# Optimization experiments

Hardware: AMD Instinct MI355X
Metric: run time of the kernel (lower is better)

Reference implementation:

```python
import jax, jax.numpy as jnp
import numpy as np


def to_float8(x, exp_bits=4, mant_bits=3):
    # Faithful port of the torch to_float8: clamp exponent, round mantissa.
    max_exp = 2 ** (exp_bits - 1) - 1
    scale = 2.0 ** mant_bits
    sign = jnp.sign(x)
    xa = jnp.abs(x)
    e = jnp.clip(jnp.floor(jnp.log2(xa + 1e-08)), -max_exp, max_exp)
    p = jnp.exp2(e)
    mant_q = jnp.round((xa / p - 1.0) * scale) / scale
    return sign * (1.0 + mant_q) * p


def setup_inputs() -> dict:
    key = jax.random.key(0)
    k0, k1, k2, k3, k4 = jax.random.split(key, 5)
    Bz, Din, L, N, Dout = 32, 512, 512, 512, 512
    u = jax.random.normal(k0, (Bz, Din, L), jnp.float32)
    # |A| < 1 for a stable length-512 recurrence
    A_diag = jax.random.uniform(k1, (N,), jnp.float32, 0.0, 0.9)
    B = jax.random.normal(k2, (N, Din), jnp.float32) * (1.0 / np.sqrt(Din))
    C = jax.random.normal(k3, (Dout, N), jnp.float32) * (1.0 / np.sqrt(N))
    D = jax.random.normal(k4, (Dout, Din), jnp.float32) * (1.0 / np.sqrt(Din))
    return {"u": u, "A_diag": A_diag, "B": B, "C": C, "D": D}


def reference(u, A_diag, B, C, D):
    int_bits, mant_bits = 4, 3
    q = lambda t: to_float8(t, int_bits, mant_bits)
    A_q = q(A_diag)[None, :]          # [1, N]
    B_q, C_q, D_q = q(B), q(C), q(D)
    Bt = B_q.T                         # [Din, N]
    # row_checksum(B_q.t()): append column of row sums -> constant across steps
    right_cs = jnp.concatenate([Bt, Bt.sum(axis=1, keepdims=True)], axis=1)  # [Din, N+1]
    Bz, Din, L = u.shape
    N = A_diag.shape[0]
    u_t = jnp.transpose(u, (2, 0, 1))  # [L, Bz, Din]

    def step(state, ut):
        # col_checksum(ut): append row of column sums
        left_cs = jnp.concatenate([ut, ut.sum(axis=0, keepdims=True)], axis=0)  # [Bz+1, Din]
        prod_cs = left_cs @ right_cs                 # [Bz+1, N+1] checksum-padded matmul
        right_term = prod_cs[:-1, :-1]               # ut @ B_q.T  (ABFT mask is discarded in forward)
        state_q = q(state * A_q + right_term)        # [Bz, N]
        y = q(state_q @ C_q.T + ut @ D_q.T)          # [Bz, Dout]
        return state_q, y

    state0 = jnp.zeros((Bz, N), u.dtype)
    _, Y = jax.lax.scan(step, state0, u_t)           # [L, Bz, Dout]
    return jnp.transpose(Y, (1, 2, 0))               # [Bz, Dout, L]
```

## Files before the change

### kernel.cpp

```cpp
#include <hip/hip_runtime.h>
#include <hip/hip_bf16.h>


#define DINX 512
#define LSEQ 512
#define NDIM 512

__device__ __forceinline__ float q8(float x) {
    float xa = fabsf(x);
    float w  = __fadd_rn(xa, 1e-8f);
    int e = (int)((__float_as_uint(w) >> 23) & 0xFFu) - 127;
    e = e < -7 ? -7 : (e > 7 ? 7 : e);
    float p    = __int_as_float((unsigned)((e + 127) << 23));
    float invp = __int_as_float((unsigned)((127 - e) << 23));
    float t  = __fmul_rn(__fsub_rn(__fmul_rn(xa, invp), 1.0f), 8.0f);
    float m  = __fmul_rn(rintf(t), 0.125f);
    float r  = __fmul_rn(__fadd_rn(1.0f, m), p);
    return copysignf(r, x);
}

__global__ void quantk(const float* __restrict__ in, float* __restrict__ out, int n) {
    int i = blockIdx.x * blockDim.x + threadIdx.x;
    if (i < n) out[i] = q8(in[i]);
}

__global__ __launch_bounds__(256) void quantT3(const float* __restrict__ B,
                                               const float* __restrict__ C,
                                               const float* __restrict__ D,
                                               float* __restrict__ Bqt,
                                               float* __restrict__ Cqt,
                                               float* __restrict__ Dqt) {
    __shared__ float tl[32][33];
    const float* in = blockIdx.z == 0 ? B : (blockIdx.z == 1 ? C : D);
    float* out      = blockIdx.z == 0 ? Bqt : (blockIdx.z == 1 ? Cqt : Dqt);
    const int r0 = blockIdx.y * 32, c0 = blockIdx.x * 32;
    const int x = threadIdx.x & 31, y = threadIdx.x >> 5;
#pragma unroll
    for (int i = 0; i < 32; i += 8)
        tl[y + i][x] = q8(in[(r0 + y + i) * 512 + c0 + x]);
    __syncthreads();
#pragma unroll
    for (int i = 0; i < 32; i += 8)
        out[(c0 + y + i) * 512 + r0 + x] = tl[x][y + i];
}

__device__ __forceinline__ void gemm_pass(const float* __restrict__ X,
                                          const float* __restrict__ W,
                                          int m0, int n0, int KTOT,
                                          float (&acc)[2][4][2][4],
                                          float (*Xs)[128], float (*Ws)[128],
                                          int tid) {
    const int tx = tid & 15, ty = tid >> 4;
    const int srow = tid >> 4, sseg4 = (tid & 15) * 4;
    const float* xp = X + (size_t)srow * 512 + m0 + sseg4;
    const float* wp = W + (size_t)srow * 512 + n0 + sseg4;
    for (int k0 = 0; k0 < KTOT; k0 += 16) {
        float4 x0 = *(const float4*)xp;
        float4 x1 = *(const float4*)(xp + 64);
        float4 w0 = *(const float4*)wp;
        float4 w1 = *(const float4*)(wp + 64);
        xp += 16 * 512; wp += 16 * 512;
        __syncthreads();
        *(float4*)&Xs[srow][sseg4]      = x0;
        *(float4*)&Xs[srow][64 + sseg4] = x1;
        *(float4*)&Ws[srow][sseg4]      = w0;
        *(float4*)&Ws[srow][64 + sseg4] = w1;
        __syncthreads();
#pragma unroll
        for (int k = 0; k < 16; ++k) {
            float a[2][4], b[2][4];
            *(float4*)&a[0][0] = *(const float4*)&Xs[k][tx * 4];
            *(float4*)&a[1][0] = *(const float4*)&Xs[k][64 + tx * 4];
            *(float4*)&b[0][0] = *(const float4*)&Ws[k][ty * 4];
            *(float4*)&b[1][0] = *(const float4*)&Ws[k][64 + ty * 4];
#pragma unroll
            for (int p = 0; p < 2; ++p)
#pragma unroll
                for (int i = 0; i < 4; ++i)
#pragma unroll
                    for (int q = 0; q < 2; ++q)
#pragma unroll
                        for (int j = 0; j < 4; ++j)
                            acc[p][i][q][j] = fmaf(a[p][i], b[q][j], acc[p][i][q][j]);
        }
    }
}

__global__ __launch_bounds__(256) void gemm_R(const float* __restrict__ u,
                                              const float* __restrict__ Bqt,
                                              float* __restrict__ R) {
    __shared__ float Xs[16][128];
    __shared__ float Ws[16][128];
    const int b  = blockIdx.z;
    const int t0 = blockIdx.x * 128, n0 = blockIdx.y * 128;
    const int tid = threadIdx.x;
    const int tx = tid & 15, ty = tid >> 4;
    const float* ub = u + (size_t)b * (DINX * LSEQ);
    float acc[2][4][2][4] = {};
    gemm_pass(ub, Bqt, t0, n0, DINX, acc, Xs, Ws, tid);
    float* Rb = R + (size_t)b * (LSEQ * NDIM);
#pragma unroll
    for (int p = 0; p < 2; ++p)
#pragma unroll
        for (int i = 0; i < 4; ++i) {
            float* row = Rb + (size_t)(t0 + p * 64 + tx * 4 + i) * NDIM + n0;
            *(float4*)(row + ty * 4)      = make_float4(acc[p][i][0][0], acc[p][i][0][1],
                                                        acc[p][i][0][2], acc[p][i][0][3]);
            *(float4*)(row + 64 + ty * 4) = make_float4(acc[p][i][1][0], acc[p][i][1][1],
                                                        acc[p][i][1][2], acc[p][i][1][3]);
        }
}

__global__ __launch_bounds__(128) void recur(const float* __restrict__ R,
                                             const float* __restrict__ Aq,
                                             float* __restrict__ S) {
    __shared__ float tile[16][132];
    const int b  = blockIdx.x;
    const int n0 = blockIdx.y * 128;
    const int n  = threadIdx.x;
    const float a = Aq[n0 + n];
    const float* Rb = R + (size_t)b * (LSEQ * NDIM) + n0;
    float* Sb = S + (size_t)b * (NDIM * LSEQ) + (size_t)n0 * LSEQ;
    float s = 0.0f;
    const int c = (n & 3) * 4;
    const int rbase = n >> 2;
    for (int t0 = 0; t0 < LSEQ; t0 += 16) {
#pragma unroll
        for (int tt = 0; tt < 16; ++tt) {
            float r = Rb[(size_t)(t0 + tt) * NDIM + n];
            s = q8(__fadd_rn(__fmul_rn(s, a), r));
            tile[tt][n] = s;
        }
        __syncthreads();
#pragma unroll
        for (int p = 0; p < 4; ++p) {
            int row = p * 32 + rbase;
            float4 v = make_float4(tile[c + 0][row], tile[c + 1][row],
                                   tile[c + 2][row], tile[c + 3][row]);
            *(float4*)(Sb + (size_t)row * LSEQ + t0 + c) = v;
        }
        __syncthreads();
    }
}

__global__ __launch_bounds__(256) void gemm_Y(const float* __restrict__ u,
                                              const float* __restrict__ S,
                                              const float* __restrict__ Cqt,
                                              const float* __restrict__ Dqt,
                                              float* __restrict__ Y) {
    __shared__ float Xs[16][128];
    __shared__ float Ws[16][128];
    const int b  = blockIdx.z;
    const int t0 = blockIdx.x * 128, o0 = blockIdx.y * 128;
    const int tid = threadIdx.x;
    const int tx = tid & 15, ty = tid >> 4;
    const float* Sb = S + (size_t)b * (NDIM * LSEQ);
    const float* ub = u + (size_t)b * (DINX * LSEQ);
    float acc[2][4][2][4] = {};
    float c1[2][4][2][4];
    gemm_pass(Sb, Cqt, t0, o0, NDIM, acc, Xs, Ws, tid);
#pragma unroll
    for (int p = 0; p < 2; ++p)
#pragma unroll
        for (int i = 0; i < 4; ++i)
#pragma unroll
            for (int q = 0; q < 2; ++q)
#pragma unroll
                for (int j = 0; j < 4; ++j) {
                    c1[p][i][q][j] = acc[p][i][q][j];
                    acc[p][i][q][j] = 0.0f;
                }
    gemm_pass(ub, Dqt, t0, o0, DINX, acc, Xs, Ws, tid);

    float* Yb = Y + (size_t)b * (NDIM * LSEQ);
#pragma unroll
    for (int q = 0; q < 2; ++q)
#pragma unroll
        for (int j = 0; j < 4; ++j) {
            float y0[4], y1[4];
#pragma unroll
            for (int i = 0; i < 4; ++i) {
                y0[i] = q8(__fadd_rn(c1[0][i][q][j], acc[0][i][q][j]));
                y1[i] = q8(__fadd_rn(c1[1][i][q][j], acc[1][i][q][j]));
            }
            float* row = Yb + (size_t)(o0 + q * 64 + ty * 4 + j) * LSEQ + t0;
            *(float4*)(row + tx * 4)      = make_float4(y0[0], y0[1], y0[2], y0[3]);
            *(float4*)(row + 64 + tx * 4) = make_float4(y1[0], y1[1], y1[2], y1[3]);
        }
}

extern "C" void kernel_launch(void* const* d_in, const int* in_sizes, int n_in,
                              void* d_out, int out_size, void* d_ws, size_t ws_size,
                              hipStream_t stream) {
    const float* u = (const float*)d_in[0];
    const float* A = (const float*)d_in[1];
    const float* B = (const float*)d_in[2];
    const float* C = (const float*)d_in[3];
    const float* D = (const float*)d_in[4];

    float* ws  = (float*)d_ws;
    float* Aq  = ws;
    float* Bqt = Aq + 512;
    float* Cqt = Bqt + 262144;
    float* Dqt = Cqt + 262144;
    float* R   = Dqt + 262144;
    float* S   = R + 8388608;
    float* Y   = (float*)d_out;

    quantk<<<2, 256, 0, stream>>>(A, Aq, 512);
    quantT3<<<dim3(16, 16, 3), 256, 0, stream>>>(B, C, D, Bqt, Cqt, Dqt);

    gemm_R<<<dim3(4, 4, 32), 256, 0, stream>>>(u, Bqt, R);
    recur<<<dim3(32, 4), 128, 0, stream>>>(R, Aq, S);
    gemm_Y<<<dim3(4, 4, 32), 256, 0, stream>>>(u, S, Cqt, Dqt, Y);
}
```

Measured before the change: 405.1 us.

## Double-buffer GEMM shared tiles and split recurrence into smaller blocks

Converts the shared GEMM inner loop to a double-buffered scheme: the next K-tile is prefetched into registers while the current tile is computed, then written to the alternate shared buffer, leaving one barrier per tile. It also halves the recurrence block width to 64 channels, doubling the block count to spread the serial scan across more compute units. The cost is doubled shared memory per GEMM block, which may lower occupancy.

```diff
diff --git a/kernel.cpp b/kernel.cpp
--- a/kernel.cpp
+++ b/kernel.cpp
@@ -44,6 +44,28 @@
         out[(c0 + y + i) * 512 + r0 + x] = tl[x][y + i];
 }
 
+__device__ __forceinline__ void tile16(const float (*Xs)[128], const float (*Ws)[128],
+                                       int base, int tx, int ty,
+                                       float (&acc)[2][4][2][4]) {
+#pragma unroll
+    for (int k = 0; k < 16; ++k) {
+        float a[2][4], b[2][4];
+        *(float4*)&a[0][0] = *(const float4*)&Xs[base + k][tx * 4];
+        *(float4*)&a[1][0] = *(const float4*)&Xs[base + k][64 + tx * 4];
+        *(float4*)&b[0][0] = *(const float4*)&Ws[base + k][ty * 4];
+        *(float4*)&b[1][0] = *(const float4*)&Ws[base + k][64 + ty * 4];
+#pragma unroll
+        for (int p = 0; p < 2; ++p)
+#pragma unroll
+            for (int i = 0; i < 4; ++i)
+#pragma unroll
+                for (int q = 0; q < 2; ++q)
+#pragma unroll
+                    for (int j = 0; j < 4; ++j)
+                        acc[p][i][q][j] = fmaf(a[p][i], b[q][j], acc[p][i][q][j]);
+    }
+}
+
 __device__ __forceinline__ void gemm_pass(const float* __restrict__ X,
                                           const float* __restrict__ W,
                                           int m0, int n0, int KTOT,
@@ -54,7 +76,8 @@
     const int srow = tid >> 4, sseg4 = (tid & 15) * 4;
     const float* xp = X + (size_t)srow * 512 + m0 + sseg4;
     const float* wp = W + (size_t)srow * 512 + n0 + sseg4;
-    for (int k0 = 0; k0 < KTOT; k0 += 16) {
+
+    {
         float4 x0 = *(const float4*)xp;
         float4 x1 = *(const float4*)(xp + 64);
         float4 w0 = *(const float4*)wp;
@@ -66,31 +89,31 @@
         *(float4*)&Ws[srow][sseg4]      = w0;
         *(float4*)&Ws[srow][64 + sseg4] = w1;
         __syncthreads();
-#pragma unroll
-        for (int k = 0; k < 16; ++k) {
-            float a[2][4], b[2][4];
-            *(float4*)&a[0][0] = *(const float4*)&Xs[k][tx * 4];
-            *(float4*)&a[1][0] = *(const float4*)&Xs[k][64 + tx * 4];
-            *(float4*)&b[0][0] = *(const float4*)&Ws[k][ty * 4];
-            *(float4*)&b[1][0] = *(const float4*)&Ws[k][64 + ty * 4];
-#pragma unroll
-            for (int p = 0; p < 2; ++p)
-#pragma unroll
-                for (int i = 0; i < 4; ++i)
-#pragma unroll
-                    for (int q = 0; q < 2; ++q)
-#pragma unroll
-                        for (int j = 0; j < 4; ++j)
-                            acc[p][i][q][j] = fmaf(a[p][i], b[q][j], acc[p][i][q][j]);
-        }
-    }
+    }
+    const int NT = KTOT >> 4;
+    for (int it = 0; it < NT - 1; ++it) {
+        float4 nx0 = *(const float4*)xp;
+        float4 nx1 = *(const float4*)(xp + 64);
+        float4 nw0 = *(const float4*)wp;
+        float4 nw1 = *(const float4*)(wp + 64);
+        xp += 16 * 512; wp += 16 * 512;
+        const int base = (it & 1) << 4;
+        tile16(Xs, Ws, base, tx, ty, acc);
+        const int nb = (base ^ 16) + srow;
+        *(float4*)&Xs[nb][sseg4]      = nx0;
+        *(float4*)&Xs[nb][64 + sseg4] = nx1;
+        *(float4*)&Ws[nb][sseg4]      = nw0;
+        *(float4*)&Ws[nb][64 + sseg4] = nw1;
+        __syncthreads();
+    }
+    tile16(Xs, Ws, ((NT - 1) & 1) << 4, tx, ty, acc);
 }
 
 __global__ __launch_bounds__(256) void gemm_R(const float* __restrict__ u,
                                               const float* __restrict__ Bqt,
                                               float* __restrict__ R) {
-    __shared__ float Xs[16][128];
-    __shared__ float Ws[16][128];
+    __shared__ float Xs[32][128];
+    __shared__ float Ws[32][128];
     const int b  = blockIdx.z;
     const int t0 = blockIdx.x * 128, n0 = blockIdx.y * 128;
     const int tid = threadIdx.x;
@@ -111,12 +134,12 @@
         }
 }
 
-__global__ __launch_bounds__(128) void recur(const float* __restrict__ R,
-                                             const float* __restrict__ Aq,
-                                             float* __restrict__ S) {
-    __shared__ float tile[16][132];
+__global__ __launch_bounds__(64) void recur(const float* __restrict__ R,
+                                            const float* __restrict__ Aq,
+                                            float* __restrict__ S) {
+    __shared__ float tile[16][68];
     const int b  = blockIdx.x;
-    const int n0 = blockIdx.y * 128;
+    const int n0 = blockIdx.y * 64;
     const int n  = threadIdx.x;
     const float a = Aq[n0 + n];
     const float* Rb = R + (size_t)b * (LSEQ * NDIM) + n0;
@@ -134,7 +157,7 @@
         __syncthreads();
 #pragma unroll
         for (int p = 0; p < 4; ++p) {
-            int row = p * 32 + rbase;
+            int row = p * 16 + rbase;
             float4 v = make_float4(tile[c + 0][row], tile[c + 1][row],
                                    tile[c + 2][row], tile[c + 3][row]);
             *(float4*)(Sb + (size_t)row * LSEQ + t0 + c) = v;
@@ -148,8 +171,8 @@
                                               const float* __restrict__ Cqt,
                                               const float* __restrict__ Dqt,
                                               float* __restrict__ Y) {
-    __shared__ float Xs[16][128];
-    __shared__ float Ws[16][128];
+    __shared__ float Xs[32][128];
+    __shared__ float Ws[32][128];
     const int b  = blockIdx.z;
     const int t0 = blockIdx.x * 128, o0 = blockIdx.y * 128;
     const int tid = threadIdx.x;
@@ -211,6 +234,6 @@
     quantT3<<<dim3(16, 16, 3), 256, 0, stream>>>(B, C, D, Bqt, Cqt, Dqt);
 
     gemm_R<<<dim3(4, 4, 32), 256, 0, stream>>>(u, Bqt, R);
-    recur<<<dim3(32, 4), 128, 0, stream>>>(R, Aq, S);
+    recur<<<dim3(32, 8), 64, 0, stream>>>(R, Aq, S);
     gemm_Y<<<dim3(4, 4, 32), 256, 0, stream>>>(u, S, Cqt, Dqt, Y);
 }
```

Measured after the change: 465.4 us. +14.9%, slower.
